# Kernel optimization log

Hardware: AMD Instinct MI355X
Metric: run time of the kernel (lower is better)

Reference implementation:

```python
import jax, jax.numpy as jnp
import numpy as np

DIM = 2048
NUM_HEADS = 16
NUM_KV_HEADS = 4
HEAD_DIM = DIM // NUM_HEADS  # 128
ROPE_BASE = 10000.0
TRAIN_SEQ_LEN = 1024
EPS = 1.1920929e-07  # torch.finfo(float32).eps, used by F.rms_norm default


def _rope_tables(seq_len, dtype=jnp.float32):
    rd = HEAD_DIM  # rope_dims defaults to full head_dim
    if seq_len > TRAIN_SEQ_LEN:
        s = seq_len / TRAIN_SEQ_LEN
        base = ROPE_BASE * s ** (rd / (rd - 2))
    else:
        base = ROPE_BASE
    inv_freq = 1.0 / base ** (jnp.arange(0, rd, 2, dtype=jnp.float32) / rd)
    t = jnp.arange(seq_len, dtype=jnp.float32)
    freqs = jnp.outer(t, inv_freq)  # [S, rd//2]
    cos = jnp.cos(freqs)[None, :, None, :].astype(dtype)  # [1,S,1,rd//2]
    sin = jnp.sin(freqs)[None, :, None, :].astype(dtype)
    return cos, sin


def _rms_norm(x):
    var = jnp.mean(jnp.square(x), axis=-1, keepdims=True)
    return x * jax.lax.rsqrt(var + EPS)


def _apply_rotary(x, cos, sin):
    h = x.shape[-1] // 2
    x1, x2 = x[..., :h], x[..., h:]
    return jnp.concatenate((x1 * cos + x2 * sin, -x1 * sin + x2 * cos), axis=-1)


def setup_inputs() -> dict:
    key = jax.random.key(0)
    ks = jax.random.split(key, 6)
    B, S = 2, 2048
    kv_dim = NUM_KV_HEADS * HEAD_DIM
    x = jax.random.normal(ks[0], (B, S, DIM), dtype=jnp.float32)
    Wq = jax.random.normal(ks[1], (DIM, DIM), dtype=jnp.float32) * 0.02
    Wk = jax.random.normal(ks[2], (kv_dim, DIM), dtype=jnp.float32) * 0.02
    Wv = jax.random.normal(ks[3], (kv_dim, DIM), dtype=jnp.float32) * 0.02
    Wo = jax.random.normal(ks[4], (DIM, DIM), dtype=jnp.float32) * 0.02
    q_gain = jnp.full((NUM_HEADS,), 1.0, dtype=jnp.float32)
    return {"x": x, "Wq": Wq, "Wk": Wk, "Wv": Wv, "Wo": Wo, "q_gain": q_gain}


def reference(x, Wq, Wk, Wv, Wo, q_gain):
    B, S, D = x.shape
    H, Hkv, Dh = NUM_HEADS, NUM_KV_HEADS, HEAD_DIM
    # QKV projections (CastedLinear, no bias)
    q = (x @ Wq.T).reshape(B, S, H, Dh)
    k = (x @ Wk.T).reshape(B, S, Hkv, Dh)
    v = (x @ Wv.T).reshape(B, S, Hkv, Dh)
    # RMSNorm over head_dim (no learned weight)
    q = _rms_norm(q)
    k = _rms_norm(k)
    # RoPE (full head_dim, NTK-scaled since S > train_seq_len)
    cos, sin = _rope_tables(S, q.dtype)
    q = _apply_rotary(q, cos, sin)
    k = _apply_rotary(k, cos, sin)
    # per-head gain on q
    q = q * q_gain.astype(q.dtype)[None, None, :, None]
    # GQA: repeat_interleave kv heads
    reps = H // Hkv
    k = jnp.repeat(k, reps, axis=2)  # [B,S,H,Dh]
    v = jnp.repeat(v, reps, axis=2)
    # causal attention
    scale = 1.0 / jnp.sqrt(jnp.asarray(Dh, dtype=q.dtype))
    scores = jnp.einsum('bqhd,bkhd->bhqk', q, k) * scale  # [B,H,S,S]
    causal = jnp.tril(jnp.ones((S, S), dtype=bool))
    scores = jnp.where(causal[None, None], scores, jnp.finfo(scores.dtype).min)
    attn = jax.nn.softmax(scores, axis=-1)
    y = jnp.einsum('bhqk,bkhd->bqhd', attn, v)  # [B,S,H,Dh]
    return y.reshape(B, S, D) @ Wo.T
```

## Files before the change

kernel.cpp:

```cpp
#include <hip/hip_runtime.h>

#define DIMSZ 2048
#define NHEAD 16
#define NKV 4
#define HD 128
#define QKVD 3072
#define SEQ 2048
#define NTOK 4096

typedef __attribute__((ext_vector_type(8))) short short8;
typedef __attribute__((ext_vector_type(4))) float f32x4;
typedef unsigned short u16;

__device__ __forceinline__ u16 f2bf(float x) {
  union { float f; unsigned u; } v; v.f = x;
  unsigned r = v.u + 0x7fffu + ((v.u >> 16) & 1u);
  return (u16)(r >> 16);
}
__device__ __forceinline__ unsigned pack_bf2(float a, float b) {
  unsigned ua = __float_as_uint(a) + 0x8000u;
  unsigned ub = __float_as_uint(b) + 0x8000u;
  return __builtin_amdgcn_perm(ub, ua, 0x07060302);
}

__device__ __forceinline__ void gl_lds16(const void* g, void* l) {
  __builtin_amdgcn_global_load_lds(
      (const __attribute__((address_space(1))) void*)g,
      (__attribute__((address_space(3))) void*)l, 16, 0, 0);
}

__global__ __launch_bounds__(256)
void castAll(const float* __restrict__ x,  const float* __restrict__ Wq,
             const float* __restrict__ Wk, const float* __restrict__ Wv,
             const float* __restrict__ Wo, u16* __restrict__ xb,
             u16* __restrict__ Wqkvb, u16* __restrict__ Wob) {
  int i = blockIdx.x * 256 + threadIdx.x;
  int f = i * 4;
  const float* src; u16* dst; int off;
  if (f < 8388608)       { src = x;  dst = xb;    off = f; }
  else if (f < 12582912) { src = Wq; dst = Wqkvb; off = f - 8388608; }
  else if (f < 13631488) { src = Wk; dst = Wqkvb + 4194304; off = f - 12582912; }
  else if (f < 14680064) { src = Wv; dst = Wqkvb + 5242880; off = f - 13631488; }
  else                   { src = Wo; dst = Wob;   off = f - 14680064; }
  float4 v = *(const float4*)(src + off);
  ushort4 o;
  o.x = f2bf(v.x); o.y = f2bf(v.y); o.z = f2bf(v.z); o.w = f2bf(v.w);
  *(ushort4*)(dst + off) = o;
}

template <bool F32OUT>
__global__ __launch_bounds__(256)
void gemm_bt(const u16* __restrict__ A, const u16* __restrict__ W,
             void* __restrict__ Cv, int M, int N, int K) {
  __shared__ u16 As[128 * 32];
  __shared__ u16 Bs[128 * 32];
  const int tid  = threadIdx.x;
  const int lane = tid & 63;
  const int wave = tid >> 6;
  const int r = lane & 15, q = lane >> 4;
  const int m0 = blockIdx.y * 128;
  const int n0 = blockIdx.x * 128;
  const int wm = (wave >> 1) * 64;
  const int wn = (wave & 1) * 64;
  const int grow = lane >> 2;
  const int gcol = (lane & 3) * 8;
  const u16* Abase = A + (long)(m0 + wave * 32 + grow) * K + gcol;
  const u16* Wbase = W + (long)(n0 + wave * 32 + grow) * K + gcol;
  u16* AsW = &As[(wave * 32) * 32];
  u16* BsW = &Bs[(wave * 32) * 32];

  f32x4 acc[4][4] = {};

  for (int k0 = 0; k0 < K; k0 += 32) {
    __syncthreads();
    gl_lds16(Abase + k0,          AsW);
    gl_lds16(Abase + 16 * K + k0, AsW + 16 * 32);
    gl_lds16(Wbase + k0,          BsW);
    gl_lds16(Wbase + 16 * K + k0, BsW + 16 * 32);
    __syncthreads();

    short8 af[4], bfr[4];
#pragma unroll
    for (int i = 0; i < 4; i++)
      af[i] = *(const short8*)&As[(wm + i * 16 + r) * 32 + q * 8];
#pragma unroll
    for (int j = 0; j < 4; j++)
      bfr[j] = *(const short8*)&Bs[(wn + j * 16 + r) * 32 + q * 8];
#pragma unroll
    for (int i = 0; i < 4; i++)
#pragma unroll
      for (int j = 0; j < 4; j++)
        acc[i][j] = __builtin_amdgcn_mfma_f32_16x16x32_bf16(af[i], bfr[j], acc[i][j], 0, 0, 0);
  }

#pragma unroll
  for (int i = 0; i < 4; i++)
#pragma unroll
    for (int j = 0; j < 4; j++) {
      int row = m0 + wm + i * 16 + q * 4;
      int col = n0 + wn + j * 16 + r;
#pragma unroll
      for (int t = 0; t < 4; t++) {
        if (F32OUT)
          ((float*)Cv)[(long)(row + t) * N + col] = acc[i][j][t];
        else
          ((u16*)Cv)[(long)(row + t) * N + col] = f2bf(acc[i][j][t]);
      }
    }
}

__global__ __launch_bounds__(256)
void prep(u16* __restrict__ qkv, const float* __restrict__ gain, float qsc,
          u16* __restrict__ vt) {
  if (blockIdx.x < 20480) {
    int gid  = blockIdx.x * 4 + (threadIdx.x >> 6);
    int lane = threadIdx.x & 63;
    int token = gid / 20;
    int idx   = gid % 20;
    int s     = token & (SEQ - 1);
    bool isq  = idx < 16;
    int off   = isq ? idx * HD : 2048 + (idx - 16) * HD;
    float psc = isq ? qsc * gain[idx & 15] : 1.0f;
    u16* p = qkv + (long)token * QKVD + off;
    union { unsigned u; float f; } c1, c2;
    c1.u = ((unsigned)p[lane]) << 16;
    c2.u = ((unsigned)p[lane + 64]) << 16;
    float x1 = c1.f, x2 = c2.f;
    float ss = x1 * x1 + x2 * x2;
#pragma unroll
    for (int d = 1; d < 64; d <<= 1) ss += __shfl_xor(ss, d);
    float rn = rsqrtf(ss * (1.0f / 128.0f) + 1.1920929e-07f) * psc;
    float lb = log2f(10000.0f) + 128.0f / 126.0f;
    float inv_freq = exp2f(-(float)lane * (lb * (1.0f / 64.0f)));
    float ang = (float)s * inv_freq;
    float sn, cs;
    sincosf(ang, &sn, &cs);
    p[lane]      = f2bf((x1 * cs + x2 * sn) * rn);
    p[lane + 64] = f2bf((-x1 * sn + x2 * cs) * rn);
  } else {
    __shared__ u16 T[128 * 72];
    int bid = blockIdx.x - 20480;
    const int k0 = (bid & 31) * 64, hkv = (bid >> 5) & 3, b = bid >> 7;
    const u16* vb = qkv + 2560;
    const int t = threadIdx.x;
    const int key = t & 63, dh0 = (t >> 6) * 32;
#pragma unroll
    for (int c = 0; c < 4; c++) {
      uint4 vv = *(const uint4*)&vb[(long)(b * SEQ + k0 + key) * QKVD + hkv * HD + dh0 + c * 8];
      u16 tmp[8];
      *(uint4*)tmp = vv;
#pragma unroll
      for (int e = 0; e < 8; e++) T[(dh0 + c * 8 + e) * 72 + key] = tmp[e];
    }
    __syncthreads();
    const int dh = t >> 1, half = t & 1;
#pragma unroll
    for (int c = 0; c < 4; c++) {
      uint4 ov = *(const uint4*)&T[dh * 72 + half * 32 + c * 8];
      *(uint4*)&vt[((long)(b * NKV + hkv) * HD + dh) * SEQ + k0 + half * 32 + c * 8] = ov;
    }
  }
}

__global__ __launch_bounds__(256, 4)
void fattn(const u16* __restrict__ qb, const u16* __restrict__ kb,
           const u16* __restrict__ vtg, u16* __restrict__ yb) {
  __shared__ u16 Ks[64 * 128];
  __shared__ u16 Vt[128 * 64];
  __shared__ u16 Ps[64 * 64];
  const int tid  = threadIdx.x;
  const int lane = tid & 63;
  const int w    = tid >> 6;
  const int r = lane & 15, q = lane >> 4;
  const int qt = 31 - (blockIdx.x >> 5);
  const int hb = blockIdx.x & 31;
  const int h  = hb >> 1;
  const int b  = hb & 1;
  const int q0 = qt * 64;
  const int hkv = h >> 2;

  long koff[4], voff[4];
  u16 *kdst[4], *vdst[4];
#pragma unroll
  for (int c = 0; c < 4; c++) {
    int gr = w * 16 + c * 4 + (lane >> 4);
    int s  = lane & 15;
    int kj = (s & 8) | ((s ^ gr) & 7);
    koff[c] = (long)gr * QKVD + hkv * HD + kj * 8;
    kdst[c] = Ks + (w * 16 + c * 4) * 128;
    int dh = (w * 4 + c) * 8 + (lane >> 3);
    int vs = lane & 7;
    int vj = (vs ^ dh) & 7;
    voff[c] = (long)dh * SEQ + vj * 8;
    vdst[c] = Vt + (w * 4 + c) * 8 * 64;
  }
  const u16* vbase = vtg + (long)(b * NKV + hkv) * HD * SEQ;

  short8 qf[4];
#pragma unroll
  for (int ks = 0; ks < 4; ks++)
    qf[ks] = *(const short8*)&qb[(long)(b * SEQ + q0 + w * 16 + r) * QKVD +
                                 h * HD + ks * 32 + q * 8];

  f32x4 oacc[8] = {};
  float l_i = 0.f;
  const int maskbase = q * 4 - w * 16 - r;
  const int psx = (r & 7) << 1;

  for (int k0 = 0; k0 <= q0; k0 += 64) {
    __syncthreads();
    const u16* kb_t = kb + (long)(b * SEQ + k0) * QKVD;
    const u16* vb_t = vbase + k0;
#pragma unroll
    for (int c = 0; c < 4; c++) {
      gl_lds16(kb_t + koff[c], kdst[c]);
      gl_lds16(vb_t + voff[c], vdst[c]);
    }
    __syncthreads();

    const bool maskit = (k0 == q0);

    f32x4 st[4] = {};
#pragma unroll
    for (int jt = 0; jt < 4; jt++)
#pragma unroll
      for (int ks = 0; ks < 4; ks++) {
        int row = jt * 16 + r;
        int j = ks * 4 + q;
        int p = (j & 8) | ((j ^ row) & 7);
        short8 kf = *(const short8*)&Ks[row * 128 + p * 8];
        st[jt] = __builtin_amdgcn_mfma_f32_16x16x32_bf16(kf, qf[ks], st[jt], 0, 0, 0);
      }

    if (maskit) {
#pragma unroll
      for (int jt = 0; jt < 4; jt++)
#pragma unroll
        for (int t = 0; t < 4; t++)
          if (jt * 16 + maskbase + t > 0) st[jt][t] = -3e38f;
    }

#pragma unroll
    for (int jt = 0; jt < 4; jt++) {
#pragma unroll
      for (int t = 0; t < 4; t++) {
        float p = exp2f(st[jt][t]);
        st[jt][t] = p;
      }
      l_i += (st[jt][0] + st[jt][1]) + (st[jt][2] + st[jt][3]);
      uint2 pk;
      pk.x = pack_bf2(st[jt][0], st[jt][1]);
      pk.y = pack_bf2(st[jt][2], st[jt][3]);
      *(uint2*)&Ps[(w * 16 + r) * 64 + ((jt * 4 + q) ^ psx) * 4] = pk;
    }
    asm volatile("s_waitcnt lgkmcnt(0)" ::: "memory");

#pragma unroll
    for (int ks = 0; ks < 2; ks++) {
      short8 pf = *(const short8*)&Ps[(w * 16 + r) * 64 + ((ks * 8 + q * 2) ^ psx) * 4];
#pragma unroll
      for (int n = 0; n < 8; n++) {
        int row = n * 16 + r;
        int j = ks * 4 + q;
        int p = (j ^ row) & 7;
        short8 vf = *(const short8*)&Vt[row * 64 + p * 8];
        oacc[n] = __builtin_amdgcn_mfma_f32_16x16x32_bf16(pf, vf, oacc[n], 0, 0, 0);
      }
    }
  }

  l_i += __shfl_xor(l_i, 16);
  l_i += __shfl_xor(l_i, 32);
  float lb4[4];
#pragma unroll
  for (int t = 0; t < 4; t++) lb4[t] = 1.0f / __shfl(l_i, q * 4 + t);
#pragma unroll
  for (int n = 0; n < 8; n++)
#pragma unroll
    for (int t = 0; t < 4; t++) {
      int row = q0 + w * 16 + q * 4 + t;
      int col = n * 16 + r;
      yb[(long)(b * SEQ + row) * DIMSZ + h * HD + col] = f2bf(oacc[n][t] * lb4[t]);
    }
}

extern "C" void kernel_launch(void* const* d_in, const int* in_sizes, int n_in,
                              void* d_out, int out_size, void* d_ws, size_t ws_size,
                              hipStream_t stream) {
  const float* x  = (const float*)d_in[0];
  const float* Wq = (const float*)d_in[1];
  const float* Wk = (const float*)d_in[2];
  const float* Wv = (const float*)d_in[3];
  const float* Wo = (const float*)d_in[4];
  const float* qg = (const float*)d_in[5];
  float* out = (float*)d_out;

  const long MB = 1024 * 1024;
  char* ws = (char*)d_ws;
  u16* xb    = (u16*)(ws + 0 * MB);
  u16* ybuf  = (u16*)(ws + 0 * MB);
  u16* Wqkvb = (u16*)(ws + 16 * MB);
  u16* Wob   = (u16*)(ws + 28 * MB);
  u16* qkv   = (u16*)(ws + 36 * MB);
  u16* vtg   = (u16*)(ws + 60 * MB);

  castAll<<<18432, 256, 0, stream>>>(x, Wq, Wk, Wv, Wo, xb, Wqkvb, Wob);

  gemm_bt<false><<<dim3(QKVD / 128, NTOK / 128), 256, 0, stream>>>(xb, Wqkvb, qkv, NTOK, QKVD, DIMSZ);

  const float qsc = 0.08838834764831845f * 1.44269504088896f;
  prep<<<20736, 256, 0, stream>>>(qkv, qg, qsc, vtg);

  fattn<<<1024, 256, 0, stream>>>(qkv, qkv + 2048, vtg, ybuf);

  gemm_bt<true><<<dim3(DIMSZ / 128, NTOK / 128), 256, 0, stream>>>(ybuf, Wob, out, NTOK, DIMSZ, DIMSZ);
}
```

Baseline: 316.2 us.

## Replace GEMM with 256x256 double-buffered, swizzled, XCD-remapped pipelined kernel

Both projection GEMMs switch from a 128x128 tile, single-buffered 256-thread kernel to a 256x256 tile, 512-thread kernel. The new kernel double-buffers LDS with K-step 64, XOR-swizzles LDS columns to avoid bank conflicts, and interleaves global-to-LDS loads with MFMA phases under manual waitcnt and barriers. It also remaps block IDs across the 8 XCDs and raises MFMA priority. The goal is to hide memory latency and raise data reuse per tile, at the cost of fewer blocks (192 and 128 tiles) and higher register and LDS use, which may underfill 256 CUs.

```diff
diff --git a/kernel.cpp b/kernel.cpp
--- a/kernel.cpp
+++ b/kernel.cpp
@@ -49,58 +49,152 @@
 }
 
 template <bool F32OUT>
-__global__ __launch_bounds__(256)
-void gemm_bt(const u16* __restrict__ A, const u16* __restrict__ W,
+__global__ __launch_bounds__(512, 2)
+void gemm256(const u16* __restrict__ A, const u16* __restrict__ W,
              void* __restrict__ Cv, int M, int N, int K) {
-  __shared__ u16 As[128 * 32];
-  __shared__ u16 Bs[128 * 32];
-  const int tid  = threadIdx.x;
-  const int lane = tid & 63;
-  const int wave = tid >> 6;
-  const int r = lane & 15, q = lane >> 4;
-  const int m0 = blockIdx.y * 128;
-  const int n0 = blockIdx.x * 128;
-  const int wm = (wave >> 1) * 64;
-  const int wn = (wave & 1) * 64;
-  const int grow = lane >> 2;
-  const int gcol = (lane & 3) * 8;
-  const u16* Abase = A + (long)(m0 + wave * 32 + grow) * K + gcol;
-  const u16* Wbase = W + (long)(n0 + wave * 32 + grow) * K + gcol;
-  u16* AsW = &As[(wave * 32) * 32];
-  u16* BsW = &Bs[(wave * 32) * 32];
-
-  f32x4 acc[4][4] = {};
-
-  for (int k0 = 0; k0 < K; k0 += 32) {
-    __syncthreads();
-    gl_lds16(Abase + k0,          AsW);
-    gl_lds16(Abase + 16 * K + k0, AsW + 16 * 32);
-    gl_lds16(Wbase + k0,          BsW);
-    gl_lds16(Wbase + 16 * K + k0, BsW + 16 * 32);
-    __syncthreads();
-
-    short8 af[4], bfr[4];
-#pragma unroll
-    for (int i = 0; i < 4; i++)
-      af[i] = *(const short8*)&As[(wm + i * 16 + r) * 32 + q * 8];
-#pragma unroll
-    for (int j = 0; j < 4; j++)
-      bfr[j] = *(const short8*)&Bs[(wn + j * 16 + r) * 32 + q * 8];
-#pragma unroll
-    for (int i = 0; i < 4; i++)
-#pragma unroll
-      for (int j = 0; j < 4; j++)
-        acc[i][j] = __builtin_amdgcn_mfma_f32_16x16x32_bf16(af[i], bfr[j], acc[i][j], 0, 0, 0);
+  __shared__ __align__(16) u16 As[2][256][64];
+  __shared__ __align__(16) u16 Bs[2][256][64];
+  const int tid = threadIdx.x;
+  const int l = tid & 63;
+  const int w = tid >> 6;
+  const int r = l & 15, q = l >> 4;
+  const int wm = (w >> 2) * 128;
+  const int wn = (w & 3) * 64;
+
+  const int nx  = N >> 8;
+  const int cpx = gridDim.x >> 3;
+  const int lid = (blockIdx.x & 7) * cpx + (blockIdx.x >> 3);
+  const int m0 = (lid / nx) << 8;
+  const int n0 = (lid % nx) << 8;
+
+  const int srow = w * 16 + (l >> 3);
+  const int scol = ((l & 7) ^ (l >> 3)) << 3;
+  const u16* Asrc = A + (long)(m0 + srow) * K + scol;
+  const u16* Bsrc = W + (long)(n0 + srow) * K + scol;
+
+  auto stA = [&](int d, int h, int kt) {
+    const u16* s = Asrc + (long)(h * 128) * K + (long)kt * 64;
+    gl_lds16(s,         &As[d][h * 128 + w * 16][0]);
+    gl_lds16(s + 8 * K, &As[d][h * 128 + w * 16 + 8][0]);
+  };
+  auto stB = [&](int d, int h, int kt) {
+    const u16* s = Bsrc + (long)(h * 128) * K + (long)kt * 64;
+    gl_lds16(s,         &Bs[d][h * 128 + w * 16][0]);
+    gl_lds16(s + 8 * K, &Bs[d][h * 128 + w * 16 + 8][0]);
+  };
+  auto lda = [&](int d, int rt, int ks) -> short8 {
+    return *(const short8*)&As[d][wm + rt * 16 + r][(((ks << 2) | q) ^ (r & 7)) << 3];
+  };
+  auto ldb = [&](int d, int ct, int ks) -> short8 {
+    return *(const short8*)&Bs[d][wn + ct * 16 + r][(((ks << 2) | q) ^ (r & 7)) << 3];
+  };
+
+  f32x4 acc[8][4] = {};
+  short8 a[4][2], b[4][2];
+
+#define MMA8(IB, JB)                                                          \
+  do {                                                                        \
+    __builtin_amdgcn_s_setprio(1);                                            \
+    _Pragma("unroll") for (int i_ = 0; i_ < 4; ++i_)                          \
+    _Pragma("unroll") for (int j_ = 0; j_ < 2; ++j_)                          \
+    _Pragma("unroll") for (int k_ = 0; k_ < 2; ++k_)                          \
+      acc[(IB) + i_][(JB) + j_] = __builtin_amdgcn_mfma_f32_16x16x32_bf16(    \
+          a[i_][k_], b[(JB) + j_][k_], acc[(IB) + i_][(JB) + j_], 0, 0, 0);   \
+    __builtin_amdgcn_s_setprio(0);                                            \
+  } while (0)
+
+#define LGKM0()                                           \
+  do {                                                    \
+    asm volatile("s_waitcnt lgkmcnt(0)" ::: "memory");    \
+    __builtin_amdgcn_sched_barrier(0);                    \
+  } while (0)
+
+  stB(0, 0, 0); stA(0, 0, 0); stB(0, 1, 0); stA(0, 1, 0);
+  stB(1, 0, 1); stA(1, 0, 1);
+  asm volatile("s_waitcnt vmcnt(4)" ::: "memory");
+  __builtin_amdgcn_s_barrier();
+
+  const int niter = K >> 7;
+  for (int it = 0; it < niter; ++it) {
+    const int kt1 = 2 * it + 1, kt2 = 2 * it + 2, kt3 = 2 * it + 3;
+    const bool more = (it + 1 < niter);
+
+#pragma unroll
+    for (int i = 0; i < 4; ++i) { a[i][0] = lda(0, i, 0); a[i][1] = lda(0, i, 1); }
+#pragma unroll
+    for (int j = 0; j < 2; ++j) { b[j][0] = ldb(0, j, 0); b[j][1] = ldb(0, j, 1); }
+    stB(1, 1, kt1);
+    __builtin_amdgcn_s_barrier();
+    LGKM0();
+    MMA8(0, 0);
+    __builtin_amdgcn_s_barrier();
+
+#pragma unroll
+    for (int j = 2; j < 4; ++j) { b[j][0] = ldb(0, j, 0); b[j][1] = ldb(0, j, 1); }
+    stA(1, 1, kt1);
+    __builtin_amdgcn_s_barrier();
+    LGKM0();
+    MMA8(0, 2);
+    __builtin_amdgcn_s_barrier();
+
+#pragma unroll
+    for (int i = 0; i < 4; ++i) { a[i][0] = lda(0, i + 4, 0); a[i][1] = lda(0, i + 4, 1); }
+    if (more) stB(0, 0, kt2);
+    __builtin_amdgcn_s_barrier();
+    LGKM0();
+    MMA8(4, 2);
+    __builtin_amdgcn_s_barrier();
+
+    if (more) stA(0, 0, kt2);
+    __builtin_amdgcn_s_barrier();
+    MMA8(4, 0);
+    if (more) asm volatile("s_waitcnt vmcnt(4)" ::: "memory");
+    else      asm volatile("s_waitcnt vmcnt(0)" ::: "memory");
+    __builtin_amdgcn_s_barrier();
+
+#pragma unroll
+    for (int i = 0; i < 4; ++i) { a[i][0] = lda(1, i, 0); a[i][1] = lda(1, i, 1); }
+#pragma unroll
+    for (int j = 0; j < 2; ++j) { b[j][0] = ldb(1, j, 0); b[j][1] = ldb(1, j, 1); }
+    if (more) stB(0, 1, kt2);
+    __builtin_amdgcn_s_barrier();
+    LGKM0();
+    MMA8(0, 0);
+    __builtin_amdgcn_s_barrier();
+
+#pragma unroll
+    for (int j = 2; j < 4; ++j) { b[j][0] = ldb(1, j, 0); b[j][1] = ldb(1, j, 1); }
+    if (more) stA(0, 1, kt2);
+    __builtin_amdgcn_s_barrier();
+    LGKM0();
+    MMA8(0, 2);
+    __builtin_amdgcn_s_barrier();
+
+#pragma unroll
+    for (int i = 0; i < 4; ++i) { a[i][0] = lda(1, i + 4, 0); a[i][1] = lda(1, i + 4, 1); }
+    if (more) stB(1, 0, kt3);
+    __builtin_amdgcn_s_barrier();
+    LGKM0();
+    MMA8(4, 2);
+    __builtin_amdgcn_s_barrier();
+
+    if (more) stA(1, 0, kt3);
+    __builtin_amdgcn_s_barrier();
+    MMA8(4, 0);
+    if (more) asm volatile("s_waitcnt vmcnt(4)" ::: "memory");
+    __builtin_amdgcn_s_barrier();
   }
-
-#pragma unroll
-  for (int i = 0; i < 4; i++)
-#pragma unroll
-    for (int j = 0; j < 4; j++) {
+#undef MMA8
+#undef LGKM0
+
+#pragma unroll
+  for (int i = 0; i < 8; ++i)
+#pragma unroll
+    for (int j = 0; j < 4; ++j) {
       int row = m0 + wm + i * 16 + q * 4;
       int col = n0 + wn + j * 16 + r;
 #pragma unroll
-      for (int t = 0; t < 4; t++) {
+      for (int t = 0; t < 4; ++t) {
         if (F32OUT)
           ((float*)Cv)[(long)(row + t) * N + col] = acc[i][j][t];
         else
@@ -306,12 +400,14 @@
 
   castAll<<<18432, 256, 0, stream>>>(x, Wq, Wk, Wv, Wo, xb, Wqkvb, Wob);
 
-  gemm_bt<false><<<dim3(QKVD / 128, NTOK / 128), 256, 0, stream>>>(xb, Wqkvb, qkv, NTOK, QKVD, DIMSZ);
+  gemm256<false><<<(QKVD / 256) * (NTOK / 256), 512, 0, stream>>>(
+      xb, Wqkvb, qkv, NTOK, QKVD, DIMSZ);
 
   const float qsc = 0.08838834764831845f * 1.44269504088896f;
   prep<<<20736, 256, 0, stream>>>(qkv, qg, qsc, vtg);
 
   fattn<<<1024, 256, 0, stream>>>(qkv, qkv + 2048, vtg, ybuf);
 
-  gemm_bt<true><<<dim3(DIMSZ / 128, NTOK / 128), 256, 0, stream>>>(ybuf, Wob, out, NTOK, DIMSZ, DIMSZ);
-}
+  gemm256<true><<<(DIMSZ / 256) * (NTOK / 256), 512, 0, stream>>>(
+      ybuf, Wob, out, NTOK, DIMSZ, DIMSZ);
+}
```

New measurement: 329.8 us. 1.04x slower.

## Replace GEMM with double-buffered swizzled 256-row tile pipelined kernel

Applied to the files above, without the earlier changes.

Replaces the simple single-buffer 128x128 GEMM with a 512-thread kernel using 256xN tiles, 64-wide K steps and double-buffered LDS. Global-to-LDS loads are interleaved with MFMA work through explicit vmcnt waits, barriers and priority hints. LDS columns are XOR-swizzled to avoid bank conflicts, and block IDs are remapped for L2 locality. The aim is to hide memory latency and raise MFMA utilisation in both projection GEMMs. In exchange it adds register pressure and a hand-tuned schedule that is tied to these shapes.

```diff
diff --git a/kernel.cpp b/kernel.cpp
--- a/kernel.cpp
+++ b/kernel.cpp
@@ -27,6 +27,14 @@
   __builtin_amdgcn_global_load_lds(
       (const __attribute__((address_space(1))) void*)g,
       (__attribute__((address_space(3))) void*)l, 16, 0, 0);
+}
+
+template <int N> __device__ __forceinline__ void vmw() {
+  asm volatile("s_waitcnt vmcnt(%0)" :: "n"(N) : "memory");
+}
+__device__ __forceinline__ void barsb() {
+  __builtin_amdgcn_s_barrier();
+  __builtin_amdgcn_sched_barrier(0);
 }
 
 __global__ __launch_bounds__(256)
@@ -48,59 +56,143 @@
   *(ushort4*)(dst + off) = o;
 }
 
-template <bool F32OUT>
-__global__ __launch_bounds__(256)
-void gemm_bt(const u16* __restrict__ A, const u16* __restrict__ W,
-             void* __restrict__ Cv, int M, int N, int K) {
-  __shared__ u16 As[128 * 32];
-  __shared__ u16 Bs[128 * 32];
-  const int tid  = threadIdx.x;
-  const int lane = tid & 63;
-  const int wave = tid >> 6;
-  const int r = lane & 15, q = lane >> 4;
-  const int m0 = blockIdx.y * 128;
-  const int n0 = blockIdx.x * 128;
-  const int wm = (wave >> 1) * 64;
-  const int wn = (wave & 1) * 64;
-  const int grow = lane >> 2;
-  const int gcol = (lane & 3) * 8;
-  const u16* Abase = A + (long)(m0 + wave * 32 + grow) * K + gcol;
-  const u16* Wbase = W + (long)(n0 + wave * 32 + grow) * K + gcol;
-  u16* AsW = &As[(wave * 32) * 32];
-  u16* BsW = &Bs[(wave * 32) * 32];
-
-  f32x4 acc[4][4] = {};
-
-  for (int k0 = 0; k0 < K; k0 += 32) {
-    __syncthreads();
-    gl_lds16(Abase + k0,          AsW);
-    gl_lds16(Abase + 16 * K + k0, AsW + 16 * 32);
-    gl_lds16(Wbase + k0,          BsW);
-    gl_lds16(Wbase + 16 * K + k0, BsW + 16 * 32);
-    __syncthreads();
-
-    short8 af[4], bfr[4];
-#pragma unroll
-    for (int i = 0; i < 4; i++)
-      af[i] = *(const short8*)&As[(wm + i * 16 + r) * 32 + q * 8];
-#pragma unroll
-    for (int j = 0; j < 4; j++)
-      bfr[j] = *(const short8*)&Bs[(wn + j * 16 + r) * 32 + q * 8];
-#pragma unroll
-    for (int i = 0; i < 4; i++)
-#pragma unroll
-      for (int j = 0; j < 4; j++)
-        acc[i][j] = __builtin_amdgcn_mfma_f32_16x16x32_bf16(af[i], bfr[j], acc[i][j], 0, 0, 0);
+template <int NCT, bool F32OUT>
+__global__ __launch_bounds__(512, 2)
+void gemmX(const u16* __restrict__ A, const u16* __restrict__ W,
+           void* __restrict__ Cv, int M, int N, int K) {
+  __shared__ __align__(16) u16 As[2][256][64];
+  __shared__ __align__(16) u16 Bs[2][NCT * 64][64];
+  const int tid = threadIdx.x;
+  const int l = tid & 63;
+  const int w = tid >> 6;
+  const int r = l & 15, q = l >> 4;
+  const int wm = (w >> 2) * 128;
+  const int wn = (w & 3) * (NCT * 16);
+
+  const int nx  = N / (NCT * 64);
+  const int cpx = gridDim.x >> 3;
+  const int lid = (blockIdx.x & 7) * cpx + (blockIdx.x >> 3);
+  const int m0 = (lid / nx) << 8;
+  const int n0 = (lid % nx) * (NCT * 64);
+
+  const int scol = ((l & 7) ^ (l >> 3)) << 3;
+  const u16* Asrc = A + (long)(m0 + w * 8 + (l >> 3)) * K + scol;
+  const u16* Bsrc = W + (long)(n0 + w * 8 + (l >> 3)) * K + scol;
+
+  auto stA = [&](int d, int u, int kt) {
+    gl_lds16(Asrc + (long)(u * 64) * K + kt * 64, &As[d][u * 64 + w * 8][0]);
+  };
+  auto stB = [&](int d, int u, int kt) {
+    gl_lds16(Bsrc + (long)(u * 64) * K + kt * 64, &Bs[d][u * 64 + w * 8][0]);
+  };
+  auto lda = [&](int d, int rt, int ks) -> short8 {
+    return *(const short8*)&As[d][wm + rt * 16 + r][(((ks << 2) | q) ^ (r & 7)) << 3];
+  };
+  auto ldb = [&](int d, int ct, int ks) -> short8 {
+    return *(const short8*)&Bs[d][wn + ct * 16 + r][(((ks << 2) | q) ^ (r & 7)) << 3];
+  };
+
+  f32x4 acc[8][NCT] = {};
+  short8 a[4][2];
+  short8 bE[NCT][2];
+  short8 bO[NCT][2];
+
+#define QUAD(i_, AB, BR)                                                      \
+  _Pragma("unroll") for (int ks_ = 0; ks_ < 2; ++ks_)                         \
+  _Pragma("unroll") for (int c_ = 0; c_ < NCT; ++c_)                          \
+    acc[(AB) + (i_)][c_] = __builtin_amdgcn_mfma_f32_16x16x32_bf16(           \
+        a[i_][ks_], BR[c_][ks_], acc[(AB) + (i_)][c_], 0, 0, 0);
+
+#pragma unroll
+  for (int u = 0; u < NCT; ++u) stB(0, u, 0);
+  stA(0, 0, 0); stA(0, 1, 0); stA(0, 2, 0); stA(0, 3, 0);
+#pragma unroll
+  for (int u = 0; u < NCT; ++u) stB(1, u, 1);
+  stA(1, 0, 1); stA(1, 2, 1);
+  vmw<NCT + 2>();
+  barsb();
+#pragma unroll
+  for (int i = 0; i < 4; ++i) { a[i][0] = lda(0, i, 0); a[i][1] = lda(0, i, 1); }
+#pragma unroll
+  for (int c = 0; c < NCT; ++c) { bE[c][0] = ldb(0, c, 0); bE[c][1] = ldb(0, c, 1); }
+
+  const int niter = K >> 7;
+  for (int it = 0; it < niter; ++it) {
+    const int kt1 = 2 * it + 1, kt2 = 2 * it + 2, kt3 = 2 * it + 3;
+    const bool more = (it + 1 < niter);
+
+    stA(1, 1, kt1); stA(1, 3, kt1);
+    __builtin_amdgcn_s_setprio(1);
+#pragma unroll
+    for (int i_ = 0; i_ < 4; ++i_) {
+      QUAD(i_, 0, bE);
+      a[i_][0] = lda(0, 4 + i_, 0); a[i_][1] = lda(0, 4 + i_, 1);
+    }
+    __builtin_amdgcn_s_setprio(0);
+    vmw<2>();
+    barsb();
+
+    if (more) {
+#pragma unroll
+      for (int u = 0; u < NCT; ++u) stB(0, u, kt2);
+      stA(0, 0, kt2); stA(0, 2, kt2);
+    }
+    __builtin_amdgcn_s_setprio(1);
+#pragma unroll
+    for (int i_ = 0; i_ < 4; ++i_) {
+      QUAD(i_, 4, bE);
+      a[i_][0] = lda(1, i_, 0); a[i_][1] = lda(1, i_, 1);
+      if (i_ == 0) {
+#pragma unroll
+        for (int c = 0; c < NCT; ++c) { bO[c][0] = ldb(1, c, 0); bO[c][1] = ldb(1, c, 1); }
+      }
+    }
+    __builtin_amdgcn_s_setprio(0);
+    if (more) vmw<NCT + 2>(); else vmw<0>();
+    barsb();
+
+    if (more) { stA(0, 1, kt2); stA(0, 3, kt2); }
+    __builtin_amdgcn_s_setprio(1);
+#pragma unroll
+    for (int i_ = 0; i_ < 4; ++i_) {
+      QUAD(i_, 0, bO);
+      a[i_][0] = lda(1, 4 + i_, 0); a[i_][1] = lda(1, 4 + i_, 1);
+    }
+    __builtin_amdgcn_s_setprio(0);
+    if (more) vmw<2>();
+    barsb();
+
+    if (more) {
+#pragma unroll
+      for (int u = 0; u < NCT; ++u) stB(1, u, kt3);
+      stA(1, 0, kt3); stA(1, 2, kt3);
+    }
+    __builtin_amdgcn_s_setprio(1);
+#pragma unroll
+    for (int i_ = 0; i_ < 4; ++i_) {
+      QUAD(i_, 4, bO);
+      if (more) {
+        a[i_][0] = lda(0, i_, 0); a[i_][1] = lda(0, i_, 1);
+        if (i_ == 0) {
+#pragma unroll
+          for (int c = 0; c < NCT; ++c) { bE[c][0] = ldb(0, c, 0); bE[c][1] = ldb(0, c, 1); }
+        }
+      }
+    }
+    __builtin_amdgcn_s_setprio(0);
+    if (more) vmw<NCT + 2>();
+    barsb();
   }
-
-#pragma unroll
-  for (int i = 0; i < 4; i++)
-#pragma unroll
-    for (int j = 0; j < 4; j++) {
+#undef QUAD
+
+#pragma unroll
+  for (int i = 0; i < 8; ++i)
+#pragma unroll
+    for (int j = 0; j < NCT; ++j) {
       int row = m0 + wm + i * 16 + q * 4;
       int col = n0 + wn + j * 16 + r;
 #pragma unroll
-      for (int t = 0; t < 4; t++) {
+      for (int t = 0; t < 4; ++t) {
         if (F32OUT)
           ((float*)Cv)[(long)(row + t) * N + col] = acc[i][j][t];
         else
@@ -306,12 +398,12 @@
 
   castAll<<<18432, 256, 0, stream>>>(x, Wq, Wk, Wv, Wo, xb, Wqkvb, Wob);
 
-  gemm_bt<false><<<dim3(QKVD / 128, NTOK / 128), 256, 0, stream>>>(xb, Wqkvb, qkv, NTOK, QKVD, DIMSZ);
+  gemmX<3, false><<<256, 512, 0, stream>>>(xb, Wqkvb, qkv, NTOK, QKVD, DIMSZ);
 
   const float qsc = 0.08838834764831845f * 1.44269504088896f;
   prep<<<20736, 256, 0, stream>>>(qkv, qg, qsc, vtg);
 
   fattn<<<1024, 256, 0, stream>>>(qkv, qkv + 2048, vtg, ybuf);
 
-  gemm_bt<true><<<dim3(DIMSZ / 128, NTOK / 128), 256, 0, stream>>>(ybuf, Wob, out, NTOK, DIMSZ, DIMSZ);
-}
+  gemmX<2, true><<<256, 512, 0, stream>>>(ybuf, Wob, out, NTOK, DIMSZ, DIMSZ);
+}
```

New measurement: 296.6 us. 1.07x faster.
